# Kernel tuning notes

Hardware: AMD Instinct MI355X
Metric: run time of the kernel (lower is better)

## Reference

```python
import jax, jax.numpy as jnp
import numpy as np

B, S, D, H = 4, 2048, 256, 8
HD = D // H  # 32
SCALE = 1.0 / jnp.sqrt(256.0)  # module divides by sqrt(256.0), NOT sqrt(head_dim)


def setup_inputs() -> dict:
    key = jax.random.key(0)
    ks = jax.random.split(key, 11)
    inp = {
        "q_in": jax.random.normal(ks[0], (B, S, D), jnp.float32),
        "k_in": jax.random.normal(ks[1], (B, S, D), jnp.float32),
        "v_in": jax.random.normal(ks[2], (B, S, D), jnp.float32),
        # causal mask, broadcastable over batch and heads; every row has >=1 one
        "mask": jnp.tril(jnp.ones((S, S), jnp.float32))[None, None, :, :],
        "Wq": jax.random.normal(ks[3], (D, D), jnp.float32) * 0.05,
        "bq": jnp.zeros((D,), jnp.float32),
        "Wk": jax.random.normal(ks[4], (D, D), jnp.float32) * 0.05,
        "bk": jnp.zeros((D,), jnp.float32),
        "Wv": jax.random.normal(ks[5], (D, D), jnp.float32) * 0.05,
        "bv": jnp.zeros((D,), jnp.float32),
        "Wo": jax.random.normal(ks[6], (D, D), jnp.float32) * 0.05,
        "bo": jnp.zeros((D,), jnp.float32),
    }
    return inp


def _mask_softmax(x, mask):
    # faithful to module: exp (no max-subtraction), remask, normalize
    e = jnp.exp(x) * mask
    return e / jnp.sum(e, axis=-1, keepdims=True)


def reference(q_in, k_in, v_in, mask, Wq, bq, Wk, bk, Wv, bv, Wo, bo):
    Q = (q_in @ Wq + bq).reshape(B, S, H, HD)
    K = (k_in @ Wk + bk).reshape(B, S, H, HD)
    V = (v_in @ Wv + bv).reshape(B, S, H, HD)
    scores = jnp.einsum("bqhd,bkhd->bhqk", Q, K) * SCALE  # [B,H,S,S]
    scores = scores * mask  # module multiplies mask into scores first
    p = _mask_softmax(scores, mask)
    attn = jnp.einsum("bhqk,bkhd->bqhd", p, V).reshape(B, S, D)
    return attn @ Wo + bo
```

## Files before the change

### kernel.cpp

```cpp
#include <hip/hip_runtime.h>
#include <hip/hip_bf16.h>

#define BATCH 4
#define S_LEN 2048
#define D_MOD 256
#define NH 8
#define HDIM 32
#define QLOG2E 0.09016844f

typedef short bf16x8 __attribute__((ext_vector_type(8)));
typedef short short4v __attribute__((ext_vector_type(4)));
typedef float f32x4 __attribute__((ext_vector_type(4)));

__device__ __forceinline__ short f2bf(float f) {
    __hip_bfloat16 h = __float2bfloat16(f);
    return *reinterpret_cast<short*>(&h);
}

__global__ __launch_bounds__(256) void wtrans_kernel(
    const float* __restrict__ Wq, const float* __restrict__ Wk,
    const float* __restrict__ Wv, const float* __restrict__ Wo,
    short* __restrict__ WT)
{
    const int wsel = blockIdx.x;
    const int k0 = blockIdx.y * 8;
    const float* W = wsel == 0 ? Wq : (wsel == 1 ? Wk : (wsel == 2 ? Wv : Wo));
    short* T = WT + (size_t)wsel * 256 * 256;
    int n = threadIdx.x;
    bf16x8 o;
    #pragma unroll
    for (int kk = 0; kk < 8; ++kk)
        o[kk] = f2bf(W[(size_t)(k0 + kk) * 256 + n]);
    *(bf16x8*)&T[(size_t)n * 256 + k0] = o;
}

__global__ __launch_bounds__(256) void qkv_proj_kernel(
    const float* __restrict__ q_in, const float* __restrict__ k_in,
    const float* __restrict__ v_in, const short* __restrict__ WT,
    const float* __restrict__ bq, const float* __restrict__ bk,
    const float* __restrict__ bv,
    short* __restrict__ Qp, short* __restrict__ Kp, short* __restrict__ Vt)
{
    __shared__ short lsA[32][264];
    const int mt = blockIdx.x;
    const int seg = blockIdx.y;
    const float* A = seg == 0 ? q_in : (seg == 1 ? k_in : v_in);
    const short* WTs = WT + (size_t)seg * 65536;
    const float* bias = seg == 0 ? bq : (seg == 1 ? bk : bv);
    const int m0 = mt * 32;
    const int tid = threadIdx.x;

    {
        const float4* A4 = (const float4*)(A + (size_t)m0 * D_MOD);
        #pragma unroll
        for (int i = 0; i < 8; ++i) {
            int f4 = tid + i * 256;
            int row = f4 >> 6, c4 = f4 & 63;
            float4 v = A4[f4];
            short4v o;
            o.x = f2bf(v.x); o.y = f2bf(v.y); o.z = f2bf(v.z); o.w = f2bf(v.w);
            *(short4v*)&lsA[row][c4 * 4] = o;
        }
    }
    __syncthreads();

    const int w = tid >> 6, l = tid & 63, g = l >> 4, r15 = l & 15;
    bf16x8 af[2][8];
    #pragma unroll
    for (int f = 0; f < 2; ++f)
        #pragma unroll
        for (int kk = 0; kk < 8; ++kk)
            af[f][kk] = *(const bf16x8*)&lsA[f * 16 + r15][kk * 32 + 8 * g];

    const int bidx = m0 >> 11;
    const int s_base = m0 & (S_LEN - 1);

    #pragma unroll
    for (int ntl = 0; ntl < 4; ++ntl) {
        int col = w * 64 + ntl * 16 + r15;
        f32x4 acc0 = {}, acc1 = {};
        #pragma unroll
        for (int kk = 0; kk < 8; ++kk) {
            bf16x8 b = *(const bf16x8*)&WTs[(size_t)col * 256 + kk * 32 + 8 * g];
            acc0 = __builtin_amdgcn_mfma_f32_16x16x32_bf16(af[0][kk], b, acc0, 0, 0, 0);
            acc1 = __builtin_amdgcn_mfma_f32_16x16x32_bf16(af[1][kk], b, acc1, 0, 0, 0);
        }
        float bval = bias[col];
        int h = col >> 5, hd = col & 31;
        if (seg == 0) {
            short* Outh = Qp + ((size_t)(bidx * NH + h) * S_LEN) * HDIM;
            #pragma unroll
            for (int r = 0; r < 4; ++r) {
                int s0 = s_base + 4 * g + r;
                Outh[(size_t)s0 * HDIM + hd]        = f2bf((acc0[r] + bval) * QLOG2E);
                Outh[(size_t)(s0 + 16) * HDIM + hd] = f2bf((acc1[r] + bval) * QLOG2E);
            }
        } else if (seg == 1) {
            short* Outh = Kp + ((size_t)(bidx * NH + h) * S_LEN) * HDIM;
            #pragma unroll
            for (int r = 0; r < 4; ++r) {
                int s0 = s_base + 4 * g + r;
                Outh[(size_t)s0 * HDIM + hd]        = f2bf(acc0[r] + bval);
                Outh[(size_t)(s0 + 16) * HDIM + hd] = f2bf(acc1[r] + bval);
            }
        } else {
            short* Vh = Vt + ((size_t)(bidx * NH + h) * HDIM + hd) * S_LEN;
            short4v o0, o1;
            #pragma unroll
            for (int r = 0; r < 4; ++r) { o0[r] = f2bf(acc0[r] + bval); o1[r] = f2bf(acc1[r] + bval); }
            size_t s = s_base + 4 * g;
            *(short4v*)&Vh[s]      = o0;
            *(short4v*)&Vh[s + 16] = o1;
        }
    }
}

__global__ __launch_bounds__(256) void attn_kernel(
    const short* __restrict__ Qp, const short* __restrict__ Kp,
    const short* __restrict__ Vt, short* __restrict__ Ab)
{
    __shared__ float comb[4][32][36];
    __shared__ float psl[4][2][16];

    const int idx = blockIdx.x;
    const int bh = 4 * (idx & 7) + ((idx >> 3) & 3);
    const int t  = idx >> 5;
    const int b = bh >> 3, hh = bh & 7;
    const int tid = threadIdx.x;
    const int w = tid >> 6, l = tid & 63, g = l >> 4, r15 = l & 15;

    const short* Qph = Qp + (size_t)bh * S_LEN * HDIM;
    const short* Kph = Kp + (size_t)bh * S_LEN * HDIM;
    const short* Vtp = Vt + (size_t)bh * HDIM * S_LEN;
    const f32x4 zero = {};

    #pragma unroll 1
    for (int ph = 0; ph < 2; ++ph) {
        const int q0 = (ph == 0 ? (63 - t) : t) * 32;
        const int ntiles = (q0 + 95) >> 6;

        bf16x8 aq0 = *(const bf16x8*)&Qph[(q0 + r15) * HDIM + 8 * g];
        bf16x8 aq1 = *(const bf16x8*)&Qph[(q0 + 16 + r15) * HDIM + 8 * g];

        f32x4 o00 = {}, o01 = {}, o10 = {}, o11 = {};
        float ps0 = 0.f, ps1 = 0.f;

        const short* kp  = Kph + w * 2048 + r15 * 32 + 8 * g;
        const short* vp0 = Vtp + r15 * S_LEN + w * 64 + 4 * g;
        const short* vp1 = vp0 + 16 * S_LEN;

        for (int kt = w; kt < ntiles; kt += 4, kp += 8192, vp0 += 256, vp1 += 256) {
            const int k0 = kt * 64;
            const bool full = (k0 + 63) <= q0;

            short4v v000 = *(const short4v*)(vp0);
            short4v v001 = *(const short4v*)(vp0 + 16);
            short4v v010 = *(const short4v*)(vp1);
            short4v v011 = *(const short4v*)(vp1 + 16);
            short4v v100 = *(const short4v*)(vp0 + 32);
            short4v v101 = *(const short4v*)(vp0 + 48);
            short4v v110 = *(const short4v*)(vp1 + 32);
            short4v v111 = *(const short4v*)(vp1 + 48);

            short4v pb[4][2];
            #pragma unroll
            for (int n = 0; n < 4; ++n) {
                bf16x8 ak = *(const bf16x8*)(kp + n * 512);
                __builtin_amdgcn_s_setprio(1);
                f32x4 s0 = __builtin_amdgcn_mfma_f32_16x16x32_bf16(ak, aq0, zero, 0, 0, 0);
                f32x4 s1 = __builtin_amdgcn_mfma_f32_16x16x32_bf16(ak, aq1, zero, 0, 0, 0);
                __builtin_amdgcn_s_setprio(0);
                if (full) {
                    #pragma unroll
                    for (int r = 0; r < 4; ++r) {
                        float e0 = exp2f(s0[r]);
                        float e1 = exp2f(s1[r]);
                        ps0 += e0; ps1 += e1;
                        pb[n][0][r] = f2bf(e0);
                        pb[n][1][r] = f2bf(e1);
                    }
                } else {
                    const int kb = k0 + n * 16 + 4 * g;
                    #pragma unroll
                    for (int r = 0; r < 4; ++r) {
                        int key = kb + r;
                        float e0 = (key <= q0 + r15)      ? exp2f(s0[r]) : 0.0f;
                        float e1 = (key <= q0 + 16 + r15) ? exp2f(s1[r]) : 0.0f;
                        ps0 += e0; ps1 += e1;
                        pb[n][0][r] = f2bf(e0);
                        pb[n][1][r] = f2bf(e1);
                    }
                }
            }

            bf16x8 pa00 = __builtin_shufflevector(pb[0][0], pb[1][0], 0,1,2,3,4,5,6,7);
            bf16x8 pa01 = __builtin_shufflevector(pb[0][1], pb[1][1], 0,1,2,3,4,5,6,7);
            bf16x8 pa10 = __builtin_shufflevector(pb[2][0], pb[3][0], 0,1,2,3,4,5,6,7);
            bf16x8 pa11 = __builtin_shufflevector(pb[2][1], pb[3][1], 0,1,2,3,4,5,6,7);
            bf16x8 bv00 = __builtin_shufflevector(v000, v001, 0,1,2,3,4,5,6,7);
            bf16x8 bv01 = __builtin_shufflevector(v010, v011, 0,1,2,3,4,5,6,7);
            bf16x8 bv10 = __builtin_shufflevector(v100, v101, 0,1,2,3,4,5,6,7);
            bf16x8 bv11 = __builtin_shufflevector(v110, v111, 0,1,2,3,4,5,6,7);

            __builtin_amdgcn_s_setprio(1);
            o00 = __builtin_amdgcn_mfma_f32_16x16x32_bf16(pa00, bv00, o00, 0, 0, 0);
            o01 = __builtin_amdgcn_mfma_f32_16x16x32_bf16(pa00, bv01, o01, 0, 0, 0);
            o10 = __builtin_amdgcn_mfma_f32_16x16x32_bf16(pa01, bv00, o10, 0, 0, 0);
            o11 = __builtin_amdgcn_mfma_f32_16x16x32_bf16(pa01, bv01, o11, 0, 0, 0);
            o00 = __builtin_amdgcn_mfma_f32_16x16x32_bf16(pa10, bv10, o00, 0, 0, 0);
            o01 = __builtin_amdgcn_mfma_f32_16x16x32_bf16(pa10, bv11, o01, 0, 0, 0);
            o10 = __builtin_amdgcn_mfma_f32_16x16x32_bf16(pa11, bv10, o10, 0, 0, 0);
            o11 = __builtin_amdgcn_mfma_f32_16x16x32_bf16(pa11, bv11, o11, 0, 0, 0);
            __builtin_amdgcn_s_setprio(0);
        }

        ps0 += __shfl_xor(ps0, 16); ps0 += __shfl_xor(ps0, 32);
        ps1 += __shfl_xor(ps1, 16); ps1 += __shfl_xor(ps1, 32);

        if (l < 16) { psl[w][0][l] = ps0; psl[w][1][l] = ps1; }
        #pragma unroll
        for (int r = 0; r < 4; ++r) {
            comb[w][4 * g + r][r15]           = o00[r];
            comb[w][4 * g + r][16 + r15]      = o01[r];
            comb[w][16 + 4 * g + r][r15]      = o10[r];
            comb[w][16 + 4 * g + r][16 + r15] = o11[r];
        }
        __syncthreads();

        {
            int q = tid >> 3, hd0 = (tid & 7) * 4;
            float ps = psl[0][q >> 4][q & 15] + psl[1][q >> 4][q & 15]
                     + psl[2][q >> 4][q & 15] + psl[3][q >> 4][q & 15];
            float inv = __fdividef(1.0f, ps);
            short4v o;
            #pragma unroll
            for (int j = 0; j < 4; ++j) {
                float v = comb[0][q][hd0 + j] + comb[1][q][hd0 + j]
                        + comb[2][q][hd0 + j] + comb[3][q][hd0 + j];
                o[j] = f2bf(v * inv);
            }
            *(short4v*)&Ab[((size_t)b * S_LEN + q0 + q) * D_MOD + hh * HDIM + hd0] = o;
        }
        if (ph == 0) __syncthreads();
    }
}

__global__ __launch_bounds__(256) void out_proj_kernel(
    const short* __restrict__ Ab, const short* __restrict__ WTo,
    const float* __restrict__ bo, float* __restrict__ out)
{
    const int m0 = blockIdx.x * 32;
    const int tid = threadIdx.x;
    const int w = tid >> 6, l = tid & 63, g = l >> 4, r15 = l & 15;

    bf16x8 af[2][8];
    #pragma unroll
    for (int f = 0; f < 2; ++f)
        #pragma unroll
        for (int kk = 0; kk < 8; ++kk)
            af[f][kk] = *(const bf16x8*)&Ab[(size_t)(m0 + f * 16 + r15) * D_MOD + kk * 32 + 8 * g];

    #pragma unroll
    for (int ntl = 0; ntl < 4; ++ntl) {
        int col = w * 64 + ntl * 16 + r15;
        f32x4 acc0 = {}, acc1 = {};
        #pragma unroll
        for (int kk = 0; kk < 8; ++kk) {
            bf16x8 bfr = *(const bf16x8*)&WTo[(size_t)col * 256 + kk * 32 + 8 * g];
            acc0 = __builtin_amdgcn_mfma_f32_16x16x32_bf16(af[0][kk], bfr, acc0, 0, 0, 0);
            acc1 = __builtin_amdgcn_mfma_f32_16x16x32_bf16(af[1][kk], bfr, acc1, 0, 0, 0);
        }
        float bval = bo[col];
        #pragma unroll
        for (int r = 0; r < 4; ++r) {
            out[(size_t)(m0 + 4 * g + r) * D_MOD + col]      = acc0[r] + bval;
            out[(size_t)(m0 + 16 + 4 * g + r) * D_MOD + col] = acc1[r] + bval;
        }
    }
}

extern "C" void kernel_launch(void* const* d_in, const int* in_sizes, int n_in,
                              void* d_out, int out_size, void* d_ws, size_t ws_size,
                              hipStream_t stream) {
    const float* q_in = (const float*)d_in[0];
    const float* k_in = (const float*)d_in[1];
    const float* v_in = (const float*)d_in[2];
    const float* Wq = (const float*)d_in[4];
    const float* bq = (const float*)d_in[5];
    const float* Wk = (const float*)d_in[6];
    const float* bk = (const float*)d_in[7];
    const float* Wv = (const float*)d_in[8];
    const float* bv = (const float*)d_in[9];
    const float* Wo = (const float*)d_in[10];
    const float* bo = (const float*)d_in[11];
    float* out = (float*)d_out;

    const size_t NTOK = (size_t)BATCH * S_LEN * D_MOD;
    short* WT = (short*)d_ws;
    short* Qp = WT + 4 * 65536;
    short* Kp = Qp + NTOK;
    short* Vt = Kp + NTOK;
    short* Ab = Vt + NTOK;

    wtrans_kernel<<<dim3(4, 32), 256, 0, stream>>>(Wq, Wk, Wv, Wo, WT);
    qkv_proj_kernel<<<dim3(256, 3), 256, 0, stream>>>(
        q_in, k_in, v_in, WT, bq, bk, bv, Qp, Kp, Vt);
    attn_kernel<<<1024, 256, 0, stream>>>(Qp, Kp, Vt, Ab);
    out_proj_kernel<<<256, 256, 0, stream>>>(Ab, WT + 3 * 65536, bo, out);
}
```

Measured before the change: 83.37 us.

## Halve row tile to 16 across projection and attention kernels for more blocks

Shrinks the per-block query/row tile from 32 to 16 rows in the QKV projection, attention and output projection kernels, doubling the grid sizes to 1536, 2048 and 512 blocks. The QKV projection now loads A rows directly from global memory into registers instead of staging them through shared memory. The aim is more parallelism and less register use per block, so the work spreads better across CUs. The cost is that K/V tiles and weight columns are reloaded twice as often, since each K/V fetch now feeds only one 16-row Q fragment.

```diff
diff --git a/kernel.cpp b/kernel.cpp
--- a/kernel.cpp
+++ b/kernel.cpp
@@ -41,36 +41,28 @@
     const float* __restrict__ bv,
     short* __restrict__ Qp, short* __restrict__ Kp, short* __restrict__ Vt)
 {
-    __shared__ short lsA[32][264];
     const int mt = blockIdx.x;
     const int seg = blockIdx.y;
     const float* A = seg == 0 ? q_in : (seg == 1 ? k_in : v_in);
     const short* WTs = WT + (size_t)seg * 65536;
     const float* bias = seg == 0 ? bq : (seg == 1 ? bk : bv);
-    const int m0 = mt * 32;
+    const int m0 = mt * 16;
     const int tid = threadIdx.x;
-
+    const int w = tid >> 6, l = tid & 63, g = l >> 4, r15 = l & 15;
+
+    bf16x8 af[8];
     {
-        const float4* A4 = (const float4*)(A + (size_t)m0 * D_MOD);
-        #pragma unroll
-        for (int i = 0; i < 8; ++i) {
-            int f4 = tid + i * 256;
-            int row = f4 >> 6, c4 = f4 & 63;
-            float4 v = A4[f4];
-            short4v o;
-            o.x = f2bf(v.x); o.y = f2bf(v.y); o.z = f2bf(v.z); o.w = f2bf(v.w);
-            *(short4v*)&lsA[row][c4 * 4] = o;
-        }
-    }
-    __syncthreads();
-
-    const int w = tid >> 6, l = tid & 63, g = l >> 4, r15 = l & 15;
-    bf16x8 af[2][8];
-    #pragma unroll
-    for (int f = 0; f < 2; ++f)
-        #pragma unroll
-        for (int kk = 0; kk < 8; ++kk)
-            af[f][kk] = *(const bf16x8*)&lsA[f * 16 + r15][kk * 32 + 8 * g];
+        const float* Ar = A + (size_t)(m0 + r15) * D_MOD + 8 * g;
+        #pragma unroll
+        for (int kk = 0; kk < 8; ++kk) {
+            float4 v0 = *(const float4*)(Ar + kk * 32);
+            float4 v1 = *(const float4*)(Ar + kk * 32 + 4);
+            af[kk][0] = f2bf(v0.x); af[kk][1] = f2bf(v0.y);
+            af[kk][2] = f2bf(v0.z); af[kk][3] = f2bf(v0.w);
+            af[kk][4] = f2bf(v1.x); af[kk][5] = f2bf(v1.y);
+            af[kk][6] = f2bf(v1.z); af[kk][7] = f2bf(v1.w);
+        }
+    }
 
     const int bidx = m0 >> 11;
     const int s_base = m0 & (S_LEN - 1);
@@ -78,12 +70,11 @@
     #pragma unroll
     for (int ntl = 0; ntl < 4; ++ntl) {
         int col = w * 64 + ntl * 16 + r15;
-        f32x4 acc0 = {}, acc1 = {};
+        f32x4 acc = {};
         #pragma unroll
         for (int kk = 0; kk < 8; ++kk) {
             bf16x8 b = *(const bf16x8*)&WTs[(size_t)col * 256 + kk * 32 + 8 * g];
-            acc0 = __builtin_amdgcn_mfma_f32_16x16x32_bf16(af[0][kk], b, acc0, 0, 0, 0);
-            acc1 = __builtin_amdgcn_mfma_f32_16x16x32_bf16(af[1][kk], b, acc1, 0, 0, 0);
+            acc = __builtin_amdgcn_mfma_f32_16x16x32_bf16(af[kk], b, acc, 0, 0, 0);
         }
         float bval = bias[col];
         int h = col >> 5, hd = col & 31;
@@ -92,25 +83,21 @@
             #pragma unroll
             for (int r = 0; r < 4; ++r) {
                 int s0 = s_base + 4 * g + r;
-                Outh[(size_t)s0 * HDIM + hd]        = f2bf((acc0[r] + bval) * QLOG2E);
-                Outh[(size_t)(s0 + 16) * HDIM + hd] = f2bf((acc1[r] + bval) * QLOG2E);
+                Outh[(size_t)s0 * HDIM + hd] = f2bf((acc[r] + bval) * QLOG2E);
             }
         } else if (seg == 1) {
             short* Outh = Kp + ((size_t)(bidx * NH + h) * S_LEN) * HDIM;
             #pragma unroll
             for (int r = 0; r < 4; ++r) {
                 int s0 = s_base + 4 * g + r;
-                Outh[(size_t)s0 * HDIM + hd]        = f2bf(acc0[r] + bval);
-                Outh[(size_t)(s0 + 16) * HDIM + hd] = f2bf(acc1[r] + bval);
+                Outh[(size_t)s0 * HDIM + hd] = f2bf(acc[r] + bval);
             }
         } else {
             short* Vh = Vt + ((size_t)(bidx * NH + h) * HDIM + hd) * S_LEN;
-            short4v o0, o1;
-            #pragma unroll
-            for (int r = 0; r < 4; ++r) { o0[r] = f2bf(acc0[r] + bval); o1[r] = f2bf(acc1[r] + bval); }
-            size_t s = s_base + 4 * g;
-            *(short4v*)&Vh[s]      = o0;
-            *(short4v*)&Vh[s + 16] = o1;
+            short4v o;
+            #pragma unroll
+            for (int r = 0; r < 4; ++r) o[r] = f2bf(acc[r] + bval);
+            *(short4v*)&Vh[s_base + 4 * g] = o;
         }
     }
 }
@@ -119,12 +106,12 @@
     const short* __restrict__ Qp, const short* __restrict__ Kp,
     const short* __restrict__ Vt, short* __restrict__ Ab)
 {
-    __shared__ float comb[4][32][36];
-    __shared__ float psl[4][2][16];
+    __shared__ float comb[4][16][36];
+    __shared__ float psl[4][16];
 
     const int idx = blockIdx.x;
     const int bh = 4 * (idx & 7) + ((idx >> 3) & 3);
-    const int t  = idx >> 5;
+    const int u  = idx >> 5;
     const int b = bh >> 3, hh = bh & 7;
     const int tid = threadIdx.x;
     const int w = tid >> 6, l = tid & 63, g = l >> 4, r15 = l & 15;
@@ -136,14 +123,13 @@
 
     #pragma unroll 1
     for (int ph = 0; ph < 2; ++ph) {
-        const int q0 = (ph == 0 ? (63 - t) : t) * 32;
-        const int ntiles = (q0 + 95) >> 6;
-
-        bf16x8 aq0 = *(const bf16x8*)&Qph[(q0 + r15) * HDIM + 8 * g];
-        bf16x8 aq1 = *(const bf16x8*)&Qph[(q0 + 16 + r15) * HDIM + 8 * g];
-
-        f32x4 o00 = {}, o01 = {}, o10 = {}, o11 = {};
-        float ps0 = 0.f, ps1 = 0.f;
+        const int q0 = (ph == 0 ? (127 - u) : u) * 16;
+        const int ntiles = (q0 + 79) >> 6;
+
+        bf16x8 aq = *(const bf16x8*)&Qph[(q0 + r15) * HDIM + 8 * g];
+
+        f32x4 o00 = {}, o01 = {};
+        float ps0 = 0.f;
 
         const short* kp  = Kph + w * 2048 + r15 * 32 + 8 * g;
         const short* vp0 = Vtp + r15 * S_LEN + w * 64 + 4 * g;
@@ -162,84 +148,67 @@
             short4v v110 = *(const short4v*)(vp1 + 32);
             short4v v111 = *(const short4v*)(vp1 + 48);
 
-            short4v pb[4][2];
+            short4v pb[4];
             #pragma unroll
             for (int n = 0; n < 4; ++n) {
                 bf16x8 ak = *(const bf16x8*)(kp + n * 512);
                 __builtin_amdgcn_s_setprio(1);
-                f32x4 s0 = __builtin_amdgcn_mfma_f32_16x16x32_bf16(ak, aq0, zero, 0, 0, 0);
-                f32x4 s1 = __builtin_amdgcn_mfma_f32_16x16x32_bf16(ak, aq1, zero, 0, 0, 0);
+                f32x4 s0 = __builtin_amdgcn_mfma_f32_16x16x32_bf16(ak, aq, zero, 0, 0, 0);
                 __builtin_amdgcn_s_setprio(0);
                 if (full) {
                     #pragma unroll
                     for (int r = 0; r < 4; ++r) {
                         float e0 = exp2f(s0[r]);
-                        float e1 = exp2f(s1[r]);
-                        ps0 += e0; ps1 += e1;
-                        pb[n][0][r] = f2bf(e0);
-                        pb[n][1][r] = f2bf(e1);
+                        ps0 += e0;
+                        pb[n][r] = f2bf(e0);
                     }
                 } else {
                     const int kb = k0 + n * 16 + 4 * g;
                     #pragma unroll
                     for (int r = 0; r < 4; ++r) {
-                        int key = kb + r;
-                        float e0 = (key <= q0 + r15)      ? exp2f(s0[r]) : 0.0f;
-                        float e1 = (key <= q0 + 16 + r15) ? exp2f(s1[r]) : 0.0f;
-                        ps0 += e0; ps1 += e1;
-                        pb[n][0][r] = f2bf(e0);
-                        pb[n][1][r] = f2bf(e1);
+                        float e0 = (kb + r <= q0 + r15) ? exp2f(s0[r]) : 0.0f;
+                        ps0 += e0;
+                        pb[n][r] = f2bf(e0);
                     }
                 }
             }
 
-            bf16x8 pa00 = __builtin_shufflevector(pb[0][0], pb[1][0], 0,1,2,3,4,5,6,7);
-            bf16x8 pa01 = __builtin_shufflevector(pb[0][1], pb[1][1], 0,1,2,3,4,5,6,7);
-            bf16x8 pa10 = __builtin_shufflevector(pb[2][0], pb[3][0], 0,1,2,3,4,5,6,7);
-            bf16x8 pa11 = __builtin_shufflevector(pb[2][1], pb[3][1], 0,1,2,3,4,5,6,7);
+            bf16x8 pa0 = __builtin_shufflevector(pb[0], pb[1], 0,1,2,3,4,5,6,7);
+            bf16x8 pa1 = __builtin_shufflevector(pb[2], pb[3], 0,1,2,3,4,5,6,7);
             bf16x8 bv00 = __builtin_shufflevector(v000, v001, 0,1,2,3,4,5,6,7);
             bf16x8 bv01 = __builtin_shufflevector(v010, v011, 0,1,2,3,4,5,6,7);
             bf16x8 bv10 = __builtin_shufflevector(v100, v101, 0,1,2,3,4,5,6,7);
             bf16x8 bv11 = __builtin_shufflevector(v110, v111, 0,1,2,3,4,5,6,7);
 
             __builtin_amdgcn_s_setprio(1);
-            o00 = __builtin_amdgcn_mfma_f32_16x16x32_bf16(pa00, bv00, o00, 0, 0, 0);
-            o01 = __builtin_amdgcn_mfma_f32_16x16x32_bf16(pa00, bv01, o01, 0, 0, 0);
-            o10 = __builtin_amdgcn_mfma_f32_16x16x32_bf16(pa01, bv00, o10, 0, 0, 0);
-            o11 = __builtin_amdgcn_mfma_f32_16x16x32_bf16(pa01, bv01, o11, 0, 0, 0);
-            o00 = __builtin_amdgcn_mfma_f32_16x16x32_bf16(pa10, bv10, o00, 0, 0, 0);
-            o01 = __builtin_amdgcn_mfma_f32_16x16x32_bf16(pa10, bv11, o01, 0, 0, 0);
-            o10 = __builtin_amdgcn_mfma_f32_16x16x32_bf16(pa11, bv10, o10, 0, 0, 0);
-            o11 = __builtin_amdgcn_mfma_f32_16x16x32_bf16(pa11, bv11, o11, 0, 0, 0);
+            o00 = __builtin_amdgcn_mfma_f32_16x16x32_bf16(pa0, bv00, o00, 0, 0, 0);
+            o01 = __builtin_amdgcn_mfma_f32_16x16x32_bf16(pa0, bv01, o01, 0, 0, 0);
+            o00 = __builtin_amdgcn_mfma_f32_16x16x32_bf16(pa1, bv10, o00, 0, 0, 0);
+            o01 = __builtin_amdgcn_mfma_f32_16x16x32_bf16(pa1, bv11, o01, 0, 0, 0);
             __builtin_amdgcn_s_setprio(0);
         }
 
         ps0 += __shfl_xor(ps0, 16); ps0 += __shfl_xor(ps0, 32);
-        ps1 += __shfl_xor(ps1, 16); ps1 += __shfl_xor(ps1, 32);
-
-        if (l < 16) { psl[w][0][l] = ps0; psl[w][1][l] = ps1; }
+
+        if (l < 16) psl[w][l] = ps0;
         #pragma unroll
         for (int r = 0; r < 4; ++r) {
-            comb[w][4 * g + r][r15]           = o00[r];
-            comb[w][4 * g + r][16 + r15]      = o01[r];
-            comb[w][16 + 4 * g + r][r15]      = o10[r];
-            comb[w][16 + 4 * g + r][16 + r15] = o11[r];
+            comb[w][4 * g + r][r15]      = o00[r];
+            comb[w][4 * g + r][16 + r15] = o01[r];
         }
         __syncthreads();
 
         {
-            int q = tid >> 3, hd0 = (tid & 7) * 4;
-            float ps = psl[0][q >> 4][q & 15] + psl[1][q >> 4][q & 15]
-                     + psl[2][q >> 4][q & 15] + psl[3][q >> 4][q & 15];
+            int q = tid >> 4, hd0 = (tid & 15) * 2;
+            float ps = psl[0][q] + psl[1][q] + psl[2][q] + psl[3][q];
             float inv = __fdividef(1.0f, ps);
-            short4v o;
-            #pragma unroll
-            for (int j = 0; j < 4; ++j) {
-                float v = comb[0][q][hd0 + j] + comb[1][q][hd0 + j]
-                        + comb[2][q][hd0 + j] + comb[3][q][hd0 + j];
-                o[j] = f2bf(v * inv);
-            }
-            *(short4v*)&Ab[((size_t)b * S_LEN + q0 + q) * D_MOD + hh * HDIM + hd0] = o;
+            float v0 = comb[0][q][hd0] + comb[1][q][hd0]
+                     + comb[2][q][hd0] + comb[3][q][hd0];
+            float v1 = comb[0][q][hd0 + 1] + comb[1][q][hd0 + 1]
+                     + comb[2][q][hd0 + 1] + comb[3][q][hd0 + 1];
+            unsigned uo = (unsigned)(unsigned short)f2bf(v0 * inv)
+                        | ((unsigned)(unsigned short)f2bf(v1 * inv) << 16);
+            *(unsigned*)&Ab[((size_t)b * S_LEN + q0 + q) * D_MOD + hh * HDIM + hd0] = uo;
         }
         if (ph == 0) __syncthreads();
     }
@@ -249,33 +218,28 @@
     const short* __restrict__ Ab, const short* __restrict__ WTo,
     const float* __restrict__ bo, float* __restrict__ out)
 {
-    const int m0 = blockIdx.x * 32;
+    const int m0 = blockIdx.x * 16;
     const int tid = threadIdx.x;
     const int w = tid >> 6, l = tid & 63, g = l >> 4, r15 = l & 15;
 
-    bf16x8 af[2][8];
-    #pragma unroll
-    for (int f = 0; f < 2; ++f)
-        #pragma unroll
-        for (int kk = 0; kk < 8; ++kk)
-            af[f][kk] = *(const bf16x8*)&Ab[(size_t)(m0 + f * 16 + r15) * D_MOD + kk * 32 + 8 * g];
+    bf16x8 af[8];
+    #pragma unroll
+    for (int kk = 0; kk < 8; ++kk)
+        af[kk] = *(const bf16x8*)&Ab[(size_t)(m0 + r15) * D_MOD + kk * 32 + 8 * g];
 
     #pragma unroll
     for (int ntl = 0; ntl < 4; ++ntl) {
         int col = w * 64 + ntl * 16 + r15;
-        f32x4 acc0 = {}, acc1 = {};
+        f32x4 acc = {};
         #pragma unroll
         for (int kk = 0; kk < 8; ++kk) {
             bf16x8 bfr = *(const bf16x8*)&WTo[(size_t)col * 256 + kk * 32 + 8 * g];
-            acc0 = __builtin_amdgcn_mfma_f32_16x16x32_bf16(af[0][kk], bfr, acc0, 0, 0, 0);
-            acc1 = __builtin_amdgcn_mfma_f32_16x16x32_bf16(af[1][kk], bfr, acc1, 0, 0, 0);
+            acc = __builtin_amdgcn_mfma_f32_16x16x32_bf16(af[kk], bfr, acc, 0, 0, 0);
         }
         float bval = bo[col];
         #pragma unroll
-        for (int r = 0; r < 4; ++r) {
-            out[(size_t)(m0 + 4 * g + r) * D_MOD + col]      = acc0[r] + bval;
-            out[(size_t)(m0 + 16 + 4 * g + r) * D_MOD + col] = acc1[r] + bval;
-        }
+        for (int r = 0; r < 4; ++r)
+            out[(size_t)(m0 + 4 * g + r) * D_MOD + col] = acc[r] + bval;
     }
 }
 
@@ -303,8 +267,8 @@
     short* Ab = Vt + NTOK;
 
     wtrans_kernel<<<dim3(4, 32), 256, 0, stream>>>(Wq, Wk, Wv, Wo, WT);
-    qkv_proj_kernel<<<dim3(256, 3), 256, 0, stream>>>(
+    qkv_proj_kernel<<<dim3(512, 3), 256, 0, stream>>>(
         q_in, k_in, v_in, WT, bq, bk, bv, Qp, Kp, Vt);
-    attn_kernel<<<1024, 256, 0, stream>>>(Qp, Kp, Vt, Ab);
-    out_proj_kernel<<<256, 256, 0, stream>>>(Ab, WT + 3 * 65536, bo, out);
-}
+    attn_kernel<<<2048, 256, 0, stream>>>(Qp, Kp, Vt, Ab);
+    out_proj_kernel<<<512, 256, 0, stream>>>(Ab, WT + 3 * 65536, bo, out);
+}
```

After: 144.5 us. 73.3% more time.
